# Performance work log

Measured on AMD Instinct MI355X. Metric: run time of the kernel, lower is better.

## Reference

```python
import jax, jax.numpy as jnp
import numpy as np

N_NODES = 100000
N_EDGES = 1600000
IN_DIM = 128
HID_DIM = 64
OUT_DIM = 1


def setup_inputs() -> dict:
    key = jax.random.key(0)
    k = jax.random.split(key, 8)
    x = jax.random.normal(k[0], (N_NODES, IN_DIM), dtype=jnp.float32)
    edge_index = jax.random.randint(k[1], (2, N_EDGES), 0, N_NODES, dtype=jnp.int64)
    # GCNConv layer 1: weight [IN, HID], bias [HID] (glorot-ish scale)
    W1 = jax.random.normal(k[2], (IN_DIM, HID_DIM), dtype=jnp.float32) / np.sqrt(IN_DIM)
    b1 = jnp.zeros((HID_DIM,), dtype=jnp.float32)
    W2 = jax.random.normal(k[3], (HID_DIM, HID_DIM), dtype=jnp.float32) / np.sqrt(HID_DIM)
    b2 = jnp.zeros((HID_DIM,), dtype=jnp.float32)
    Wfc = jax.random.normal(k[4], (HID_DIM, OUT_DIM), dtype=jnp.float32) / np.sqrt(HID_DIM)
    bfc = jnp.zeros((OUT_DIM,), dtype=jnp.float32)
    return {"x": x, "edge_index": edge_index, "W1": W1, "b1": b1,
            "W2": W2, "b2": b2, "Wfc": Wfc, "bfc": bfc}


def _gcn_norm(edge_index, n_nodes):
    # PyG GCNConv default: add self-loops, symmetric normalization.
    src, dst = edge_index[0], edge_index[1]
    loop = jnp.arange(n_nodes, dtype=src.dtype)
    src = jnp.concatenate([src, loop])
    dst = jnp.concatenate([dst, loop])
    deg = jax.ops.segment_sum(jnp.ones_like(dst, dtype=jnp.float32), dst,
                              num_segments=n_nodes)
    deg_isqrt = jax.lax.rsqrt(deg)  # deg >= 1 thanks to self-loops
    norm = deg_isqrt[src] * deg_isqrt[dst]  # [E+N]
    return src, dst, norm


def _gcn_conv(x, src, dst, norm, W, b, n_nodes):
    h = x @ W                      # [N, D_out] dense transform first (D_out <= D_in)
    msg = h[src] * norm[:, None]   # gather + normalize  [E+N, D_out]
    out = jax.ops.segment_sum(msg, dst, num_segments=n_nodes)  # scatter-add
    return out + b


def reference(x, edge_index, W1, b1, W2, b2, Wfc, bfc):
    n = x.shape[0]
    src, dst, norm = _gcn_norm(edge_index, n)
    h = jax.nn.relu(_gcn_conv(x, src, dst, norm, W1, b1, n))
    h = jax.nn.relu(_gcn_conv(h, src, dst, norm, W2, b2, n))
    return h @ Wfc + bfc  # [N, 1]
```

## Files before the change

### kernel.cpp

```cpp
#include <hip/hip_runtime.h>


#define IN_DIM 128
#define HID 64
#define B1 256
#define MAXNC 512

typedef unsigned int uint;
typedef unsigned short ushort;
typedef __attribute__((ext_vector_type(8))) short short8;
typedef __attribute__((ext_vector_type(4))) float f32x4;

__device__ inline uint pack_bf16x2(float a, float b) {
    uint ua = __builtin_bit_cast(uint, a);
    uint ub = __builtin_bit_cast(uint, b);
    ua += 0x7fffu + ((ua >> 16) & 1u);
    ub += 0x7fffu + ((ub >> 16) & 1u);
    return (ua >> 16) | (ub & 0xffff0000u);
}
__device__ inline float bf_lo(uint g) { return __builtin_bit_cast(float, g << 16); }
__device__ inline float bf_hi(uint g) { return __builtin_bit_cast(float, g & 0xffff0000u); }
__device__ inline uint rne_hi_bits(float a) {
    uint u = __builtin_bit_cast(uint, a);
    return (u + 0x7fffu + ((u >> 16) & 1u)) & 0xffff0000u;
}
__device__ inline float bitf(uint u) { return __builtin_bit_cast(float, u); }

__global__ __launch_bounds__(512) void hist1(const int* __restrict__ dst,
                                             int* __restrict__ ghist,
                                             int E, int NC, int chunk) {
    __shared__ int h[MAXNC];
    int t = threadIdx.x, blk = blockIdx.x;
    if (t < NC) h[t] = 0;
    __syncthreads();
    int s = blk * chunk, e = min(E, s + chunk);
    for (int i = s + t; i < e; i += 512) atomicAdd(&h[dst[i] >> 8], 1);
    __syncthreads();
    if (t < NC) ghist[(size_t)t * B1 + blk] = h[t];
}

__global__ __launch_bounds__(256) void scan_p1(const int* __restrict__ a,
                                               int* __restrict__ bsum, int M) {
    int i = blockIdx.x * 256 + threadIdx.x;
    int v = (i < M) ? a[i] : 0;
#pragma unroll
    for (int o = 32; o; o >>= 1) v += __shfl_down(v, o, 64);
    __shared__ int ws[4];
    int lane = threadIdx.x & 63, wid = threadIdx.x >> 6;
    if (lane == 0) ws[wid] = v;
    __syncthreads();
    if (threadIdx.x == 0) bsum[blockIdx.x] = ws[0] + ws[1] + ws[2] + ws[3];
}

__global__ __launch_bounds__(512) void scan_p2(const int* __restrict__ bsum,
                                               int* __restrict__ boff,
                                               int* __restrict__ row_off,
                                               int nb, int N,
                                               const float* __restrict__ W1f,
                                               const float* __restrict__ W2f,
                                               ushort* __restrict__ w1h,
                                               ushort* __restrict__ w1l,
                                               ushort* __restrict__ w2h,
                                               ushort* __restrict__ w2l) {
    int t = threadIdx.x;
    {
        int c = t & 63;
        int kb1 = (t >> 6) * 16;
#pragma unroll 4
        for (int kk = 0; kk < 16; ++kk) {
            int k = kb1 + kk;
            float v = W1f[k * 64 + c];
            uint rh = rne_hi_bits(v);
            w1h[c * 128 + k] = (ushort)(rh >> 16);
            w1l[c * 128 + k] = (ushort)(rne_hi_bits(v - bitf(rh)) >> 16);
        }
        int kb2 = (t >> 6) * 8;
#pragma unroll 4
        for (int kk = 0; kk < 8; ++kk) {
            int k = kb2 + kk;
            float v = W2f[k * 64 + c];
            uint rh = rne_hi_bits(v);
            w2h[c * 64 + k] = (ushort)(rh >> 16);
            w2l[c * 64 + k] = (ushort)(rne_hi_bits(v - bitf(rh)) >> 16);
        }
    }
    __shared__ int s[512];
    int v = (t < nb) ? bsum[t] : 0;
    s[t] = v;
    __syncthreads();
#pragma unroll
    for (int o = 1; o < 512; o <<= 1) {
        int add = (t >= o) ? s[t - o] : 0;
        __syncthreads();
        s[t] += add;
        __syncthreads();
    }
    if (t < nb) boff[t] = s[t] - v;
    if (t == nb - 1) row_off[N] = s[t];
}

__global__ __launch_bounds__(256) void scan_p3(int* __restrict__ a,
                                               const int* __restrict__ boff, int M) {
    __shared__ int s[256];
    int i = blockIdx.x * 256 + threadIdx.x;
    int t = threadIdx.x;
    int d = (i < M) ? a[i] : 0;
    s[t] = d;
    __syncthreads();
#pragma unroll
    for (int o = 1; o < 256; o <<= 1) {
        int add = (t >= o) ? s[t - o] : 0;
        __syncthreads();
        s[t] += add;
        __syncthreads();
    }
    if (i < M) a[i] = s[t] - d + boff[blockIdx.x];
}

__global__ __launch_bounds__(512) void scatter1(const int* __restrict__ src,
                                                const int* __restrict__ dst,
                                                const int* __restrict__ goff,
                                                uint* __restrict__ pairs,
                                                int E, int NC, int chunk) {
    __shared__ int cur[MAXNC];
    int t = threadIdx.x, blk = blockIdx.x;
    if (t < NC) cur[t] = goff[(size_t)t * B1 + blk];
    __syncthreads();
    int s = blk * chunk, e = min(E, s + chunk);
    for (int i = s + t; i < e; i += 512) {
        int d = dst[i];
        int p = atomicAdd(&cur[d >> 8], 1);
        pairs[p] = ((uint)src[i] << 8) | (uint)(d & 255);
    }
}

__global__ __launch_bounds__(256) void build_csr(const uint* __restrict__ pairs,
                                                 const int* __restrict__ goff,
                                                 int* __restrict__ row_off,
                                                 float* __restrict__ disqrt,
                                                 int* __restrict__ col,
                                                 int E, int NC, int N) {
    __shared__ int h[256], cur[256];
    __shared__ int ws[4], wsoff[4];
    int b = blockIdx.x, t = threadIdx.x;
    int base = goff[(size_t)b * B1];
    int next = (b + 1 < NC) ? goff[(size_t)(b + 1) * B1] : E;
    h[t] = 0;
    __syncthreads();
    for (int i = base + t; i < next; i += 256)
        atomicAdd(&h[pairs[i] & 255u], 1);
    __syncthreads();
    int deg = h[t];
    int incl = deg;
#pragma unroll
    for (int o = 1; o < 64; o <<= 1) {
        int u = __shfl_up(incl, o, 64);
        if ((t & 63) >= o) incl += u;
    }
    if ((t & 63) == 63) ws[t >> 6] = incl;
    __syncthreads();
    if (t == 0) {
        int run = 0;
#pragma unroll
        for (int i = 0; i < 4; ++i) { wsoff[i] = run; run += ws[i]; }
    }
    __syncthreads();
    int excl = wsoff[t >> 6] + incl - deg;
    cur[t] = base + excl;
    int node = (b << 8) + t;
    if (node < N) {
        row_off[node] = base + excl;
        disqrt[node]  = rsqrtf((float)(deg + 1));
    }
    __syncthreads();
    for (int i = base + t; i < next; i += 256) {
        uint p = pairs[i];
        int pos = atomicAdd(&cur[p & 255u], 1);
        col[pos] = (int)(p >> 8);
    }
}

template <int K, bool SPLIT>
__global__ __launch_bounds__(256) void gemm_mfma(const void* __restrict__ Xv,
                                                 const ushort* __restrict__ WHt,
                                                 const ushort* __restrict__ WLt,
                                                 const float* __restrict__ disqrt,
                                                 uint* __restrict__ Tsb, int n) {
    __shared__ ushort XH[128 * 40];
    __shared__ ushort WH[64 * 40];
    __shared__ ushort WL[64 * 40];
    __shared__ ushort XL[SPLIT ? 128 * 40 : 64];

    const int tid = threadIdx.x;
    const int m0  = blockIdx.x * 128;
    const float* Xf = (const float*)Xv;
    const char*  Xb = (const char*)Xv;

    const int wc = tid >> 2, wslot = tid & 3;
    const char* wh_g = (const char*)WHt + wc * (K * 2) + wslot * 16;
    const char* wl_g = (const char*)WLt + wc * (K * 2) + wslot * 16;

    constexpr int NL = SPLIT ? 4 : 2;
    int xr[NL], xk[NL];
#pragma unroll
    for (int i = 0; i < NL; ++i) {
        int f = tid + i * 256;
        if (SPLIT) { xr[i] = f >> 3; xk[i] = f & 7; }
        else       { xr[i] = f >> 2; xk[i] = f & 3; }
    }

    const float4 z4 = make_float4(0.f, 0.f, 0.f, 0.f);
    const uint4  zu = make_uint4(0u, 0u, 0u, 0u);
    float4 gx[NL];
    uint4  gxb[NL];
    uint4  gwh, gwl;
#pragma unroll
    for (int i = 0; i < NL; ++i) {
        int row = m0 + xr[i];
        if (SPLIT) gx[i]  = (row < n) ? *(const float4*)(Xf + (size_t)row * K + 4 * xk[i]) : z4;
        else       gxb[i] = (row < n) ? *(const uint4*)(Xb + (size_t)row * (K * 2) + xk[i] * 16) : zu;
    }
    gwh = *(const uint4*)wh_g;
    gwl = *(const uint4*)wl_g;

    f32x4 acc[2][4] = {};
    const int l   = tid & 63, wv = tid >> 6;
    const int lr  = l & 15;
    const int kob = (l >> 4) * 16;

    for (int kc = 0;;) {
        if (SPLIT) {
#pragma unroll
            for (int i = 0; i < NL; ++i) {
                float a = gx[i].x, b = gx[i].y, c = gx[i].z, d = gx[i].w;
                uint rha = rne_hi_bits(a), rhb = rne_hi_bits(b);
                uint rhc = rne_hi_bits(c), rhd = rne_hi_bits(d);
                uint2 hh, ll;
                hh.x = (rha >> 16) | (rhb & 0xffff0000u);
                hh.y = (rhc >> 16) | (rhd & 0xffff0000u);
                ll.x = pack_bf16x2(a - bitf(rha), b - bitf(rhb));
                ll.y = pack_bf16x2(c - bitf(rhc), d - bitf(rhd));
                *(uint2*)((char*)XH + xr[i] * 80 + xk[i] * 8) = hh;
                *(uint2*)((char*)XL + xr[i] * 80 + xk[i] * 8) = ll;
            }
        } else {
#pragma unroll
            for (int i = 0; i < NL; ++i)
                *(uint4*)((char*)XH + xr[i] * 80 + xk[i] * 16) = gxb[i];
        }
        *(uint4*)((char*)WH + wc * 80 + wslot * 16) = gwh;
        *(uint4*)((char*)WL + wc * 80 + wslot * 16) = gwl;
        __syncthreads();

        kc += 32;
        const bool more = kc < K;
        if (more) {
#pragma unroll
            for (int i = 0; i < NL; ++i) {
                int row = m0 + xr[i];
                if (SPLIT) gx[i]  = (row < n) ? *(const float4*)(Xf + (size_t)row * K + kc + 4 * xk[i]) : z4;
                else       gxb[i] = (row < n) ? *(const uint4*)(Xb + (size_t)row * (K * 2) + kc * 2 + xk[i] * 16) : zu;
            }
            gwh = *(const uint4*)(wh_g + kc * 2);
            gwl = *(const uint4*)(wl_g + kc * 2);
        }

        short8 xh0 = *(const short8*)((const char*)XH + (wv * 32 + 0 + lr) * 80 + kob);
        short8 xh1 = *(const short8*)((const char*)XH + (wv * 32 + 16 + lr) * 80 + kob);
        short8 xl0, xl1;
        if (SPLIT) {
            xl0 = *(const short8*)((const char*)XL + (wv * 32 + 0 + lr) * 80 + kob);
            xl1 = *(const short8*)((const char*)XL + (wv * 32 + 16 + lr) * 80 + kob);
        }
#pragma unroll
        for (int nn = 0; nn < 4; ++nn) {
            short8 wh = *(const short8*)((const char*)WH + (nn * 16 + lr) * 80 + kob);
            short8 wl = *(const short8*)((const char*)WL + (nn * 16 + lr) * 80 + kob);
            acc[0][nn] = __builtin_amdgcn_mfma_f32_16x16x32_bf16(wh, xh0, acc[0][nn], 0, 0, 0);
            acc[1][nn] = __builtin_amdgcn_mfma_f32_16x16x32_bf16(wh, xh1, acc[1][nn], 0, 0, 0);
            acc[0][nn] = __builtin_amdgcn_mfma_f32_16x16x32_bf16(wl, xh0, acc[0][nn], 0, 0, 0);
            acc[1][nn] = __builtin_amdgcn_mfma_f32_16x16x32_bf16(wl, xh1, acc[1][nn], 0, 0, 0);
            if (SPLIT) {
                acc[0][nn] = __builtin_amdgcn_mfma_f32_16x16x32_bf16(wh, xl0, acc[0][nn], 0, 0, 0);
                acc[1][nn] = __builtin_amdgcn_mfma_f32_16x16x32_bf16(wh, xl1, acc[1][nn], 0, 0, 0);
            }
        }
        if (!more) break;
        __syncthreads();
    }

#pragma unroll
    for (int m = 0; m < 2; ++m) {
        int node = m0 + wv * 32 + m * 16 + lr;
        if (node < n) {
            float dq = disqrt[node];
#pragma unroll
            for (int nn = 0; nn < 4; ++nn) {
                f32x4 a = acc[m][nn];
                uint2 pk;
                pk.x = pack_bf16x2(a[0] * dq, a[1] * dq);
                pk.y = pack_bf16x2(a[2] * dq, a[3] * dq);
                *(uint2*)((char*)Tsb + (size_t)node * 128 + nn * 32 + (l >> 4) * 8) = pk;
            }
        }
    }
}

template <bool FUSE_FC>
__global__ __launch_bounds__(256) void agg_kernel(const uint* __restrict__ Tsb,
                                                  const int* __restrict__ row_off,
                                                  const int* __restrict__ col,
                                                  const float* __restrict__ disqrt,
                                                  const float* __restrict__ bias,
                                                  const float* __restrict__ wfc,
                                                  const float* __restrict__ bfc,
                                                  uint* __restrict__ outb,
                                                  float* __restrict__ outf,
                                                  int node0, int nhi) {
    int node = node0 + blockIdx.x * 4 + (threadIdx.x >> 6);
    if (node >= nhi) return;
    int lane = threadIdx.x & 63;
    int o = lane >> 3;
    int p = lane & 7;
    float acc[8] = {};
    if (o == 0) {
        uint4 g = *(const uint4*)(Tsb + (size_t)node * 32 + 4 * p);
        acc[0] = bf_lo(g.x); acc[1] = bf_hi(g.x);
        acc[2] = bf_lo(g.y); acc[3] = bf_hi(g.y);
        acc[4] = bf_lo(g.z); acc[5] = bf_hi(g.z);
        acc[6] = bf_lo(g.w); acc[7] = bf_hi(g.w);
    }
    int beg = __builtin_amdgcn_readfirstlane(row_off[node]);
    int end = __builtin_amdgcn_readfirstlane(row_off[node + 1]);
    for (int batch = beg; batch < end; batch += 64) {
        int bn = min(64, end - batch);
        int cv = 0;
        if (batch + lane < end) cv = col[batch + lane];
        int j = 0;
        for (; j + 16 <= bn; j += 16) {
            int s0 = __shfl(cv, j + o, 64);
            int s1 = __shfl(cv, j + 8 + o, 64);
            uint4 g0 = *(const uint4*)(Tsb + (size_t)s0 * 32 + 4 * p);
            uint4 g1 = *(const uint4*)(Tsb + (size_t)s1 * 32 + 4 * p);
            acc[0] += bf_lo(g0.x); acc[1] += bf_hi(g0.x);
            acc[2] += bf_lo(g0.y); acc[3] += bf_hi(g0.y);
            acc[4] += bf_lo(g0.z); acc[5] += bf_hi(g0.z);
            acc[6] += bf_lo(g0.w); acc[7] += bf_hi(g0.w);
            acc[0] += bf_lo(g1.x); acc[1] += bf_hi(g1.x);
            acc[2] += bf_lo(g1.y); acc[3] += bf_hi(g1.y);
            acc[4] += bf_lo(g1.z); acc[5] += bf_hi(g1.z);
            acc[6] += bf_lo(g1.w); acc[7] += bf_hi(g1.w);
        }
        for (; j < bn; j += 8) {
            int idx = j + o;
            int s = __shfl(cv, idx & 63, 64);
            uint4 g = *(const uint4*)(Tsb + (size_t)s * 32 + 4 * p);
            if (idx < bn) {
                acc[0] += bf_lo(g.x); acc[1] += bf_hi(g.x);
                acc[2] += bf_lo(g.y); acc[3] += bf_hi(g.y);
                acc[4] += bf_lo(g.z); acc[5] += bf_hi(g.z);
                acc[6] += bf_lo(g.w); acc[7] += bf_hi(g.w);
            }
        }
    }
#pragma unroll
    for (int k = 0; k < 8; ++k) {
        acc[k] += __shfl_xor(acc[k], 8, 64);
        acc[k] += __shfl_xor(acc[k], 16, 64);
        acc[k] += __shfl_xor(acc[k], 32, 64);
    }
    float dq = disqrt[node];
    float4 bv0 = *(const float4*)(bias + 8 * p);
    float4 bv1 = *(const float4*)(bias + 8 * p + 4);
    float r[8];
    r[0] = fmaxf(acc[0] * dq + bv0.x, 0.f);
    r[1] = fmaxf(acc[1] * dq + bv0.y, 0.f);
    r[2] = fmaxf(acc[2] * dq + bv0.z, 0.f);
    r[3] = fmaxf(acc[3] * dq + bv0.w, 0.f);
    r[4] = fmaxf(acc[4] * dq + bv1.x, 0.f);
    r[5] = fmaxf(acc[5] * dq + bv1.y, 0.f);
    r[6] = fmaxf(acc[6] * dq + bv1.z, 0.f);
    r[7] = fmaxf(acc[7] * dq + bv1.w, 0.f);
    if (!FUSE_FC) {
        if (o == 0) {
            uint4 pk;
            pk.x = pack_bf16x2(r[0], r[1]);
            pk.y = pack_bf16x2(r[2], r[3]);
            pk.z = pack_bf16x2(r[4], r[5]);
            pk.w = pack_bf16x2(r[6], r[7]);
            *(uint4*)(outb + (size_t)node * 32 + 4 * p) = pk;
        }
    } else {
        float4 wv0 = *(const float4*)(wfc + 8 * p);
        float4 wv1 = *(const float4*)(wfc + 8 * p + 4);
        float v = r[0] * wv0.x + r[1] * wv0.y + r[2] * wv0.z + r[3] * wv0.w +
                  r[4] * wv1.x + r[5] * wv1.y + r[6] * wv1.z + r[7] * wv1.w;
        v += __shfl_down(v, 4, 64);
        v += __shfl_down(v, 2, 64);
        v += __shfl_down(v, 1, 64);
        if (lane == 0) outf[node] = v + bfc[0];
    }
}

extern "C" void kernel_launch(void* const* d_in, const int* in_sizes, int n_in,
                              void* d_out, int out_size, void* d_ws, size_t ws_size,
                              hipStream_t stream) {
    const float* x   = (const float*)d_in[0];
    const int*   ei  = (const int*)d_in[1];
    const float* W1  = (const float*)d_in[2];
    const float* b1  = (const float*)d_in[3];
    const float* W2  = (const float*)d_in[4];
    const float* b2  = (const float*)d_in[5];
    const float* Wfc = (const float*)d_in[6];
    const float* bfc = (const float*)d_in[7];
    float* out = (float*)d_out;

    const int N = in_sizes[0] / IN_DIM;
    const int E = in_sizes[1] / 2;
    const int* src = ei;
    const int* dst = ei + E;
    const int NC    = (N + 255) >> 8;
    const int chunk = (E + B1 - 1) / B1;
    const int M     = NC * B1;
    const int NBs   = (M + 255) / 256;

    char* w = (char*)d_ws;
    auto alloc = [&](size_t bytes) {
        void* p = (void*)w;
        w += (bytes + 255) & ~(size_t)255;
        return p;
    };
    int*   row_off = (int*)alloc((size_t)(N + 1) * 4);
    float* disqrt  = (float*)alloc((size_t)N * 4);
    int*   goff    = (int*)alloc((size_t)NC * B1 * 4);
    int*   bsum    = (int*)alloc(512 * 4);
    int*   boff    = (int*)alloc(512 * 4);
    int*   col     = (int*)alloc((size_t)E * 4);
    ushort* w1h    = (ushort*)alloc(64 * 128 * 2);
    ushort* w1l    = (ushort*)alloc(64 * 128 * 2);
    ushort* w2h    = (ushort*)alloc(64 * 64 * 2);
    ushort* w2l    = (ushort*)alloc(64 * 64 * 2);
    size_t scrA = (size_t)E * 4, scrB = (size_t)N * HID * 2;
    void*  scr  = alloc(scrA > scrB ? scrA : scrB);
    uint*  h1b  = (uint*)alloc((size_t)N * HID * 2);
    uint*  pairs = (uint*)scr;
    uint*  Tsb   = (uint*)scr;

    hist1<<<B1, 512, 0, stream>>>(dst, goff, E, NC, chunk);
    scan_p1<<<NBs, 256, 0, stream>>>(goff, bsum, M);
    scan_p2<<<1, 512, 0, stream>>>(bsum, boff, row_off, NBs, N,
                                   W1, W2, w1h, w1l, w2h, w2l);
    scan_p3<<<NBs, 256, 0, stream>>>(goff, boff, M);
    scatter1<<<B1, 512, 0, stream>>>(src, dst, goff, pairs, E, NC, chunk);
    build_csr<<<NC, 256, 0, stream>>>(pairs, goff, row_off, disqrt, col, E, NC, N);

    gemm_mfma<IN_DIM, true><<<(N + 127) / 128, 256, 0, stream>>>(
        x, w1h, w1l, disqrt, Tsb, N);
    agg_kernel<false><<<(N + 3) / 4, 256, 0, stream>>>(Tsb, row_off, col, disqrt,
                                                       b1, nullptr, nullptr,
                                                       h1b, nullptr, 0, N);

    gemm_mfma<HID, false><<<(N + 127) / 128, 256, 0, stream>>>(
        h1b, w2h, w2l, disqrt, Tsb, N);
    agg_kernel<true><<<(N + 3) / 4, 256, 0, stream>>>(Tsb, row_off, col, disqrt,
                                                      b2, Wfc, bfc,
                                                      nullptr, out, 0, N);
}
```

Before: 265.5 us.

## Fuse block-sum into single-block scan and split aggregation into two launches

Result: slower. 283.8 us (+6.9%).

```diff
diff --git a/kernel.cpp b/kernel.cpp
--- a/kernel.cpp
+++ b/kernel.cpp
@@ -39,29 +39,16 @@
     if (t < NC) ghist[(size_t)t * B1 + blk] = h[t];
 }
 
-__global__ __launch_bounds__(256) void scan_p1(const int* __restrict__ a,
-                                               int* __restrict__ bsum, int M) {
-    int i = blockIdx.x * 256 + threadIdx.x;
-    int v = (i < M) ? a[i] : 0;
-#pragma unroll
-    for (int o = 32; o; o >>= 1) v += __shfl_down(v, o, 64);
-    __shared__ int ws[4];
-    int lane = threadIdx.x & 63, wid = threadIdx.x >> 6;
-    if (lane == 0) ws[wid] = v;
-    __syncthreads();
-    if (threadIdx.x == 0) bsum[blockIdx.x] = ws[0] + ws[1] + ws[2] + ws[3];
-}
-
-__global__ __launch_bounds__(512) void scan_p2(const int* __restrict__ bsum,
-                                               int* __restrict__ boff,
-                                               int* __restrict__ row_off,
-                                               int nb, int N,
-                                               const float* __restrict__ W1f,
-                                               const float* __restrict__ W2f,
-                                               ushort* __restrict__ w1h,
-                                               ushort* __restrict__ w1l,
-                                               ushort* __restrict__ w2h,
-                                               ushort* __restrict__ w2l) {
+__global__ __launch_bounds__(512) void scan_p12(const int* __restrict__ a,
+                                                int* __restrict__ boff,
+                                                int* __restrict__ row_off,
+                                                int M, int N,
+                                                const float* __restrict__ W1f,
+                                                const float* __restrict__ W2f,
+                                                ushort* __restrict__ w1h,
+                                                ushort* __restrict__ w1l,
+                                                ushort* __restrict__ w2h,
+                                                ushort* __restrict__ w2l) {
     int t = threadIdx.x;
     {
         int c = t & 63;
@@ -84,8 +71,21 @@
             w2l[c * 64 + k] = (ushort)(rne_hi_bits(v - bitf(rh)) >> 16);
         }
     }
+    const int nb = (M + 255) >> 8;
+    int v = 0;
+    if (t < nb) {
+        int base = t * 256, end = min(M, base + 256);
+        const int4* p4 = (const int4*)(a + base);
+        int4 sa = make_int4(0, 0, 0, 0);
+        int q4 = (end - base) >> 2;
+        for (int k = 0; k < q4; ++k) {
+            int4 q = p4[k];
+            sa.x += q.x; sa.y += q.y; sa.z += q.z; sa.w += q.w;
+        }
+        v = sa.x + sa.y + sa.z + sa.w;
+        for (int r = base + (q4 << 2); r < end; ++r) v += a[r];
+    }
     __shared__ int s[512];
-    int v = (t < nb) ? bsum[t] : 0;
     s[t] = v;
     __syncthreads();
 #pragma unroll
@@ -433,7 +433,6 @@
     int*   row_off = (int*)alloc((size_t)(N + 1) * 4);
     float* disqrt  = (float*)alloc((size_t)N * 4);
     int*   goff    = (int*)alloc((size_t)NC * B1 * 4);
-    int*   bsum    = (int*)alloc(512 * 4);
     int*   boff    = (int*)alloc(512 * 4);
     int*   col     = (int*)alloc((size_t)E * 4);
     ushort* w1h    = (ushort*)alloc(64 * 128 * 2);
@@ -447,22 +446,29 @@
     uint*  Tsb   = (uint*)scr;
 
     hist1<<<B1, 512, 0, stream>>>(dst, goff, E, NC, chunk);
-    scan_p1<<<NBs, 256, 0, stream>>>(goff, bsum, M);
-    scan_p2<<<1, 512, 0, stream>>>(bsum, boff, row_off, NBs, N,
-                                   W1, W2, w1h, w1l, w2h, w2l);
+    scan_p12<<<1, 512, 0, stream>>>(goff, boff, row_off, M, N,
+                                    W1, W2, w1h, w1l, w2h, w2l);
     scan_p3<<<NBs, 256, 0, stream>>>(goff, boff, M);
     scatter1<<<B1, 512, 0, stream>>>(src, dst, goff, pairs, E, NC, chunk);
     build_csr<<<NC, 256, 0, stream>>>(pairs, goff, row_off, disqrt, col, E, NC, N);
 
+    const int H = ((N + 7) / 8) * 4;
+
     gemm_mfma<IN_DIM, true><<<(N + 127) / 128, 256, 0, stream>>>(
         x, w1h, w1l, disqrt, Tsb, N);
-    agg_kernel<false><<<(N + 3) / 4, 256, 0, stream>>>(Tsb, row_off, col, disqrt,
+    agg_kernel<false><<<(H + 3) / 4, 256, 0, stream>>>(Tsb, row_off, col, disqrt,
                                                        b1, nullptr, nullptr,
-                                                       h1b, nullptr, 0, N);
+                                                       h1b, nullptr, 0, H);
+    agg_kernel<false><<<(N - H + 3) / 4, 256, 0, stream>>>(Tsb, row_off, col, disqrt,
+                                                           b1, nullptr, nullptr,
+                                                           h1b, nullptr, H, N);
 
     gemm_mfma<HID, false><<<(N + 127) / 128, 256, 0, stream>>>(
         h1b, w2h, w2l, disqrt, Tsb, N);
-    agg_kernel<true><<<(N + 3) / 4, 256, 0, stream>>>(Tsb, row_off, col, disqrt,
+    agg_kernel<true><<<(H + 3) / 4, 256, 0, stream>>>(Tsb, row_off, col, disqrt,
                                                       b2, Wfc, bfc,
-                                                      nullptr, out, 0, N);
-}
+                                                      nullptr, out, 0, H);
+    agg_kernel<true><<<(N - H + 3) / 4, 256, 0, stream>>>(Tsb, row_off, col, disqrt,
+                                                          b2, Wfc, bfc,
+                                                          nullptr, out, H, N);
+}
```
